# Performance work log

Measured on AMD Instinct MI355X. Metric: run time of the kernel, lower is better.

## Reference

```python
import jax, jax.numpy as jnp
import numpy as np

N, D, HW, FF, DD = 128, 256, 28, 2048, 64
NP_ = D * DD  # num_params = hidden_dim * dim_dynamic = 16384
NH_SELF, NH_ENC = 8, 4


def _conv(x, w, b, stride=1):
    y = jax.lax.conv_general_dilated(x, w, (stride, stride), ((1, 1), (1, 1)),
                                     dimension_numbers=('NCHW', 'OIHW', 'NCHW'))
    return y + b[None, :, None, None]


def _bn(x, g, b):
    # eval-mode BatchNorm2d with running_mean=0, running_var=1
    return x * g[None, :, None, None] + b[None, :, None, None]


def _ln(x, g, b, eps=1e-5):
    m = x.mean(-1, keepdims=True)
    v = ((x - m) ** 2).mean(-1, keepdims=True)
    return (x - m) / jnp.sqrt(v + eps) * g + b


def _mha(x, qkv_w, qkv_b, out_w, out_b, nh):
    # x: (S, B, D) seq-first, like torch MultiheadAttention
    S, B, Dm = x.shape
    dh = Dm // nh
    q, k, v = jnp.split(x @ qkv_w.T + qkv_b, 3, axis=-1)
    q = q.reshape(S, B, nh, dh) * (1.0 / np.sqrt(dh))
    k = k.reshape(S, B, nh, dh)
    v = v.reshape(S, B, nh, dh)
    a = jax.nn.softmax(jnp.einsum('sbhd,tbhd->bhst', q, k), axis=-1)
    o = jnp.einsum('bhst,tbhd->sbhd', a, v).reshape(S, B, Dm)
    return o @ out_w.T + out_b


def _up2(x):
    return jnp.repeat(jnp.repeat(x, 2, axis=2), 2, axis=3)


def _pe(max_len, d):
    pos = jnp.arange(max_len, dtype=jnp.float32)[:, None]
    div = jnp.exp(jnp.arange(0, d, 2, dtype=jnp.float32) * (-np.log(10000.0) / d))
    pe = jnp.zeros((max_len, d), jnp.float32)
    pe = pe.at[:, 0::2].set(jnp.sin(pos * div)).at[:, 1::2].set(jnp.cos(pos * div))
    return pe[:, None, :]  # (max_len, 1, d)


def _forward(roi_features, pro_features, enc_conv_w, enc_conv_b, enc_bn_g, enc_bn_b, attn_qkv_w, attn_qkv_b, attn_out_w, attn_out_b, norm1_g, norm1_b, norm2_g, norm2_b, norm3_g, norm3_b, dyn_w, dyn_b, dnorm1_g, dnorm1_b, dnorm2_g, dnorm2_b, lin1_w, lin1_b, lin2_w, lin2_b, te_qkv_w, te_qkv_b, te_out_w, te_out_b, te_ln1_g, te_ln1_b, te_ln2_g, te_ln2_b, te_ff1_w, te_ff1_b, te_ff2_w, te_ff2_b, rec_conv_w, rec_conv_b, rec_bn_g, rec_bn_b, detA_w, detA_b, det_bnA_g, det_bnA_b, detB_w, detB_b, det_final_w, det_final_b, det_final_bn_g, det_final_bn_b):
    n = roi_features.shape[0]
    h4 = HW // 4
    # ---- k_encoder: two stride-2 conv+BN+ReLU, 28->14->7 ----
    feats_pyr = []
    k = roi_features
    for i in range(2):
        k = jax.nn.relu(_bn(_conv(k, enc_conv_w[i], enc_conv_b[i], stride=2), enc_bn_g[i], enc_bn_b[i]))
        feats_pyr.append(k)
    k = k.reshape(n, D, h4 * h4).transpose(2, 0, 1)  # (49, N, D)
    # ---- self-attention over query tokens ----
    pro = pro_features.reshape(-1, pro_features.shape[-2], D).transpose(1, 0, 2)  # (nq, bs*nf, D)
    pro = _ln(pro + _mha(pro, attn_qkv_w, attn_qkv_b, attn_out_w, attn_out_b, NH_SELF), norm1_g, norm1_b)
    pro = pro.transpose(1, 0, 2).reshape(1, -1, D)  # (1, N, D)
    # ---- DynamicConv_v2 instance interaction ----
    feats = k.transpose(1, 0, 2)  # (N, 49, D)
    params = (pro @ dyn_w.T + dyn_b).transpose(1, 0, 2)  # (N, 1, 2*NP_)
    p1 = params[:, :, :NP_].reshape(-1, D, DD)   # (N, D, 64)
    p2 = params[:, :, NP_:].reshape(-1, DD, D)   # (N, 64, D)
    f = jax.nn.elu(_ln(jnp.einsum('nsc,ncd->nsd', feats, p1), dnorm1_g, dnorm1_b))
    f = jax.nn.elu(_ln(jnp.einsum('nsd,ndc->nsc', f, p2), dnorm2_g, dnorm2_b))  # (N, 49, D)
    pro = feats + f
    obj = _ln(pro, norm2_g, norm2_b)
    # ---- FFN (ELU activation) ----
    obj2 = jax.nn.elu(obj @ lin1_w.T + lin1_b) @ lin2_w.T + lin2_b
    obj = _ln(obj + obj2, norm3_g, norm3_b)
    # ---- pos encoding + 3-layer TransformerEncoder (post-norm, relu, nhead=4) ----
    obj = obj.transpose(1, 0, 2)  # (49, N, D)
    obj = obj + _pe(h4 * h4, D)
    for l in range(3):
        a = _mha(obj, te_qkv_w[l], te_qkv_b[l], te_out_w[l], te_out_b[l], NH_ENC)
        obj = _ln(obj + a, te_ln1_g[l], te_ln1_b[l])
        ff = jax.nn.relu(obj @ te_ff1_w[l].T + te_ff1_b[l]) @ te_ff2_w[l].T + te_ff2_b[l]
        obj = _ln(obj + ff, te_ln2_g[l], te_ln2_b[l])
    obj = obj.transpose(1, 2, 0).reshape(n, D, h4, h4)
    kmap = k.transpose(1, 2, 0).reshape(n, D, h4, h4)
    # ---- gated rec/det decoder pyramid ----
    k_rec = kmap * jax.nn.sigmoid(obj)
    k_rec = jax.nn.relu(_bn(_conv(_up2(k_rec), rec_conv_w[0], rec_conv_b[0]), rec_bn_g[0], rec_bn_b[0])) + feats_pyr[0]
    k_det = _conv(jax.nn.relu(_bn(_conv(_up2(obj), detA_w[0], detA_b[0]), det_bnA_g[0], det_bnA_b[0])), detB_w[0], detB_b[0]) + feats_pyr[0]
    k_rec = k_rec * jax.nn.sigmoid(k_det)
    k_rec = jax.nn.relu(_bn(_conv(_up2(k_rec), rec_conv_w[1], rec_conv_b[1]), rec_bn_g[1], rec_bn_b[1])) + roi_features
    k_det = _conv(jax.nn.relu(_bn(_conv(_up2(k_det), detA_w[1], detA_b[1]), det_bnA_g[1], det_bnA_b[1])), detB_w[1], detB_b[1]) + roi_features
    k_rec = k_rec * jax.nn.sigmoid(k_det)
    # final decoder_layer: Upsample to (28,28) is identity here, then conv+BN+ReLU
    k_rec = jax.nn.relu(_bn(_conv(k_rec, det_final_w, det_final_b), det_final_bn_g, det_final_bn_b))
    return k_rec.reshape(n, D, HW * HW).transpose(0, 2, 1)  # (N, 784, D)


def setup_inputs():
    keys = iter(jax.random.split(jax.random.key(0), 80))
    def rn(shape, s=0.02):
        return jax.random.normal(next(keys), shape, jnp.float32) * s
    d = {
        'roi_features': jax.random.normal(next(keys), (N, D, HW, HW), jnp.float32),
        'pro_features': jax.random.normal(next(keys), (1, 1, N, D), jnp.float32),
        'gt_masks': jax.random.normal(next(keys), (N, HW, HW), jnp.float32),
        'enc_conv_w': rn((2, D, D, 3, 3)), 'enc_conv_b': rn((2, D)),
        'enc_bn_g': jnp.ones((2, D)), 'enc_bn_b': jnp.zeros((2, D)),
        'attn_qkv_w': rn((3 * D, D)), 'attn_qkv_b': rn((3 * D,)),
        'attn_out_w': rn((D, D)), 'attn_out_b': rn((D,)),
        'norm1_g': jnp.ones((D,)), 'norm1_b': jnp.zeros((D,)),
        'norm2_g': jnp.ones((D,)), 'norm2_b': jnp.zeros((D,)),
        'norm3_g': jnp.ones((D,)), 'norm3_b': jnp.zeros((D,)),
        'dyn_w': rn((2 * NP_, D)), 'dyn_b': rn((2 * NP_,)),
        'dnorm1_g': jnp.ones((DD,)), 'dnorm1_b': jnp.zeros((DD,)),
        'dnorm2_g': jnp.ones((D,)), 'dnorm2_b': jnp.zeros((D,)),
        'lin1_w': rn((FF, D)), 'lin1_b': rn((FF,)),
        'lin2_w': rn((D, FF)), 'lin2_b': rn((D,)),
        'te_qkv_w': rn((3, 3 * D, D)), 'te_qkv_b': rn((3, 3 * D)),
        'te_out_w': rn((3, D, D)), 'te_out_b': rn((3, D)),
        'te_ln1_g': jnp.ones((3, D)), 'te_ln1_b': jnp.zeros((3, D)),
        'te_ln2_g': jnp.ones((3, D)), 'te_ln2_b': jnp.zeros((3, D)),
        'te_ff1_w': rn((3, FF, D)), 'te_ff1_b': rn((3, FF)),
        'te_ff2_w': rn((3, D, FF)), 'te_ff2_b': rn((3, D)),
        'rec_conv_w': rn((2, D, D, 3, 3)), 'rec_conv_b': rn((2, D)),
        'rec_bn_g': jnp.ones((2, D)), 'rec_bn_b': jnp.zeros((2, D)),
        'detA_w': rn((2, D, D, 3, 3)), 'detA_b': rn((2, D)),
        'det_bnA_g': jnp.ones((2, D)), 'det_bnA_b': jnp.zeros((2, D)),
        'detB_w': rn((2, D, D, 3, 3)), 'detB_b': rn((2, D)),
        'det_final_w': rn((D, D, 3, 3)), 'det_final_b': rn((D,)),
        'det_final_bn_g': jnp.ones((D,)), 'det_final_bn_b': jnp.zeros((D,)),
    }
    return d


def reference(roi_features, pro_features, gt_masks, enc_conv_w, enc_conv_b, enc_bn_g, enc_bn_b, attn_qkv_w, attn_qkv_b, attn_out_w, attn_out_b, norm1_g, norm1_b, norm2_g, norm2_b, norm3_g, norm3_b, dyn_w, dyn_b, dnorm1_g, dnorm1_b, dnorm2_g, dnorm2_b, lin1_w, lin1_b, lin2_w, lin2_b, te_qkv_w, te_qkv_b, te_out_w, te_out_b, te_ln1_g, te_ln1_b, te_ln2_g, te_ln2_b, te_ff1_w, te_ff1_b, te_ff2_w, te_ff2_b, rec_conv_w, rec_conv_b, rec_bn_g, rec_bn_b, detA_w, detA_b, det_bnA_g, det_bnA_b, detB_w, detB_b, det_final_w, det_final_b, det_final_bn_g, det_final_bn_b):
    # gt_masks is only consumed by the (truncated) SequencePredictor head; unused here
    return _forward(roi_features, pro_features, enc_conv_w, enc_conv_b, enc_bn_g, enc_bn_b, attn_qkv_w, attn_qkv_b, attn_out_w, attn_out_b, norm1_g, norm1_b, norm2_g, norm2_b, norm3_g, norm3_b, dyn_w, dyn_b, dnorm1_g, dnorm1_b, dnorm2_g, dnorm2_b, lin1_w, lin1_b, lin2_w, lin2_b, te_qkv_w, te_qkv_b, te_out_w, te_out_b, te_ln1_g, te_ln1_b, te_ln2_g, te_ln2_b, te_ff1_w, te_ff1_b, te_ff2_w, te_ff2_b, rec_conv_w, rec_conv_b, rec_bn_g, rec_bn_b, detA_w, detA_b, det_bnA_g, det_bnA_b, detB_w, detB_b, det_final_w, det_final_b, det_final_bn_g, det_final_bn_b)
```

## Files before the change

### kernel.cpp

```cpp
#include <hip/hip_runtime.h>
#include <hip/hip_bf16.h>
#include <string.h>

typedef __hip_bfloat16 bf16;
typedef short bf16x8 __attribute__((ext_vector_type(8)));
typedef float f32x16 __attribute__((ext_vector_type(16)));

__device__ __forceinline__ float b2f(bf16 v){ return __bfloat162float(v); }
__device__ __forceinline__ bf16  f2b(float v){ return __float2bfloat16(v); }
__device__ __forceinline__ unsigned short f2bu(float v){
  union { bf16 b; unsigned short u; } x; x.b = __float2bfloat16(v); return x.u;
}
__device__ __forceinline__ float ldf(const float* p, size_t i){ return p[i]; }
__device__ __forceinline__ float ldf(const bf16*  p, size_t i){ return b2f(p[i]); }

__device__ __forceinline__ float2 block_stats256(float x, float* sred){
  float v = x;
  #pragma unroll
  for (int o = 32; o; o >>= 1) v += __shfl_xor(v, o);
  int w = threadIdx.x >> 6;
  if ((threadIdx.x & 63) == 0) sred[w] = v;
  __syncthreads();
  float mean = (sred[0] + sred[1] + sred[2] + sred[3]) * (1.f/256.f);
  __syncthreads();
  float d = x - mean;
  v = d * d;
  #pragma unroll
  for (int o = 32; o; o >>= 1) v += __shfl_xor(v, o);
  if ((threadIdx.x & 63) == 0) sred[w] = v;
  __syncthreads();
  float var = (sred[0] + sred[1] + sred[2] + sred[3]) * (1.f/256.f);
  __syncthreads();
  return make_float2(mean, var);
}

__global__ __launch_bounds__(256) void probe_k(const bf16* __restrict__ buf,
                                               unsigned long long len, float* score){
  __shared__ float sred[4];
  unsigned long long stride = len / 256ull; if (!stride) stride = 1;
  unsigned long long i = (unsigned long long)threadIdx.x * stride;
  if (i >= len) i = len - 1;
  float v = fabsf(b2f(buf[i]));
  #pragma unroll
  for (int o = 32; o; o >>= 1) v = fmaxf(v, __shfl_xor(v, o));
  if ((threadIdx.x & 63) == 0) sred[threadIdx.x >> 6] = v;
  __syncthreads();
  if (threadIdx.x == 0)
    score[0] = fmaxf(fmaxf(sred[0], sred[1]), fmaxf(sred[2], sred[3]));
}

__global__ void verdict_k(const float* score, int nstage, float* out){
  if (threadIdx.x == 0 && blockIdx.x == 0){
    for (int i = 0; i < nstage; i++){
      float s = score[i];
      if (!(s > 1e-8f)){
        float sent = 1000.f + 40.f * i;
        for (int j = 0; j < 64; j++) out[j] = sent;
        return;
      }
    }
  }
}

__global__ __launch_bounds__(256) void troi_k(const float* __restrict__ roi,
                                              bf16* __restrict__ o){
  __shared__ float tile[64][65];
  int n = blockIdx.z, c0 = blockIdx.y * 64, p0 = blockIdx.x * 64;
  int a = threadIdx.x & 63, bq = threadIdx.x >> 6;
  #pragma unroll
  for (int cs = bq; cs < 64; cs += 4){
    int p = p0 + a;
    tile[cs][a] = (p < 784) ? roi[((size_t)n*256 + c0 + cs)*784 + p] : 0.f;
  }
  __syncthreads();
  #pragma unroll
  for (int ps = bq; ps < 64; ps += 4){
    int p = p0 + ps;
    if (p < 784) o[((size_t)n*784 + p)*256 + c0 + a] = f2b(tile[a][ps]);
  }
}

__global__ __launch_bounds__(256) void wtrans_k(const float* __restrict__ w,
                                                bf16* __restrict__ o){
  int co = blockIdx.x, t = threadIdx.x;
  const float* wp = w + (size_t)co * 2304 + (size_t)t * 9;
  #pragma unroll
  for (int tap = 0; tap < 9; tap++)
    o[(size_t)co * 2304 + tap * 256 + t] = f2b(wp[tap]);
}

template<typename T>
__device__ __forceinline__ void stage32(const T* __restrict__ src, bool valid,
                                        char* ldsrow, int ckbase, int swz){
  __align__(16) unsigned short h[32];
  if (valid){
    if constexpr (sizeof(T) == 4){
      #pragma unroll
      for (int i = 0; i < 8; i++){
        float4 f = reinterpret_cast<const float4*>(src)[i];
        h[i*4+0] = f2bu(f.x); h[i*4+1] = f2bu(f.y);
        h[i*4+2] = f2bu(f.z); h[i*4+3] = f2bu(f.w);
      }
    } else {
      #pragma unroll
      for (int i = 0; i < 4; i++)
        reinterpret_cast<uint4*>(h)[i] = reinterpret_cast<const uint4*>(src)[i];
    }
  } else {
    #pragma unroll
    for (int i = 0; i < 4; i++)
      reinterpret_cast<uint4*>(h)[i] = make_uint4(0u,0u,0u,0u);
  }
  #pragma unroll
  for (int i = 0; i < 4; i++)
    *reinterpret_cast<uint4*>(ldsrow + ((ckbase + i*16) ^ swz)) =
        reinterpret_cast<uint4*>(h)[i];
}

__device__ __forceinline__ void mfma_step64(const char* asb, const char* bsb,
                                            int wr, int wc, int lane,
                                            f32x16 (&acc)[2][2]){
  int l31 = lane & 31;
  int lsw = (l31 & 7) << 4;
  int hi  = (lane >> 5) << 4;
  #pragma unroll
  for (int kb = 0; kb < 4; kb++){
    int cb = (kb*32 + hi) ^ lsw;
    bf16x8 a0 = *reinterpret_cast<const bf16x8*>(asb + (wr      + l31)*128 + cb);
    bf16x8 a1 = *reinterpret_cast<const bf16x8*>(asb + (wr + 32 + l31)*128 + cb);
    bf16x8 b0 = *reinterpret_cast<const bf16x8*>(bsb + (wc      + l31)*128 + cb);
    bf16x8 b1 = *reinterpret_cast<const bf16x8*>(bsb + (wc + 32 + l31)*128 + cb);
    acc[0][0] = __builtin_amdgcn_mfma_f32_32x32x16_bf16(a0, b0, acc[0][0], 0, 0, 0);
    acc[0][1] = __builtin_amdgcn_mfma_f32_32x32x16_bf16(a0, b1, acc[0][1], 0, 0, 0);
    acc[1][0] = __builtin_amdgcn_mfma_f32_32x32x16_bf16(a1, b0, acc[1][0], 0, 0, 0);
    acc[1][1] = __builtin_amdgcn_mfma_f32_32x32x16_bf16(a1, b1, acc[1][1], 0, 0, 0);
  }
}

template<int ACT, typename TA>
__global__ __launch_bounds__(256) void gemm_mfma_k(
    const TA* __restrict__ A, const float* __restrict__ W,
    const float* __restrict__ bias, bf16* __restrict__ C,
    int M, int N, int K)
{
  __shared__ __align__(16) unsigned short As[8192];
  __shared__ __align__(16) unsigned short Bs[8192];
  int t = threadIdx.x;
  int n0 = blockIdx.x * 128, m0 = blockIdx.y * 128;
  int lane = t & 63, wave = t >> 6;
  int wr = (wave >> 1) * 64, wc = (wave & 1) * 64;
  int sr = t >> 1, sk = (t & 1) * 32;
  int swz = (sr & 7) << 4;
  char* asb = (char*)As; char* bsb = (char*)Bs;
  char* arow = asb + sr*128; char* brow = bsb + sr*128;
  f32x16 acc[2][2];
  #pragma unroll
  for (int i = 0; i < 2; i++)
    #pragma unroll
    for (int j = 0; j < 2; j++)
      #pragma unroll
      for (int r = 0; r < 16; r++) acc[i][j][r] = 0.f;

  const TA*    ap = A + (size_t)(m0 + sr) * K + sk;
  const float* wp = W + (size_t)(n0 + sr) * K + sk;
  #pragma unroll 1
  for (int k0 = 0; k0 < K; k0 += 64){
    stage32(ap + k0, true, arow, sk*2, swz);
    stage32(wp + k0, true, brow, sk*2, swz);
    __syncthreads();
    mfma_step64(asb, bsb, wr, wc, lane, acc);
    __syncthreads();
  }
  int l31 = lane & 31;
  int rbase = m0 + wr + ((lane >> 5) << 2);
  #pragma unroll
  for (int j = 0; j < 2; j++){
    int n = n0 + wc + j*32 + l31;
    float bv = bias ? bias[n] : 0.f;
    #pragma unroll
    for (int i = 0; i < 2; i++){
      #pragma unroll
      for (int r = 0; r < 16; r++){
        int row = rbase + i*32 + (r & 3) + ((r >> 2) << 3);
        float v = acc[i][j][r] + bv;
        if (ACT == 1) v = fmaxf(v, 0.f);
        if (ACT == 2) v = v > 0.f ? v : (__expf(v) - 1.f);
        C[(size_t)row * N + n] = f2b(v);
      }
    }
  }
}

template<int Ho,int Wo,int Hi,int Wi,int UP2,int STRIDE,
         int HAS_BN,int RELU,int RES_MODE,int GATE,int WOUT,int OUTF>
__global__ __launch_bounds__(256) void conv_mfma_k(
    const bf16* __restrict__ in, const bf16* __restrict__ wTl,
    const float* __restrict__ cbias,
    const float* __restrict__ bng, const float* __restrict__ bnb,
    const void* __restrict__ res, bf16* __restrict__ gate,
    void* __restrict__ out)
{
  constexpr int HWo = Ho * Wo;
  __shared__ __align__(16) unsigned short As[8192];
  __shared__ __align__(16) unsigned short Bs[8192];
  int t = threadIdx.x;
  int co0 = blockIdx.x * 128;
  int gp0 = blockIdx.y * 128;
  int lane = t & 63, wave = t >> 6;
  int wr = (wave >> 1) * 64, wc = (wave & 1) * 64;
  int sr = t >> 1, sk = (t & 1) * 32;
  int swz = (sr & 7) << 4;
  char* asb = (char*)As; char* bsb = (char*)Bs;
  char* arow = asb + sr*128; char* brow = bsb + sr*128;

  int gp = gp0 + sr;
  int n  = gp / HWo;
  int p  = gp - n * HWo;
  int oy = p / Wo, ox = p - oy * Wo;
  const bf16* wrow = wTl + (size_t)(co0 + sr) * 2304;

  f32x16 acc[2][2];
  #pragma unroll
  for (int i = 0; i < 2; i++)
    #pragma unroll
    for (int j = 0; j < 2; j++)
      #pragma unroll
      for (int r = 0; r < 16; r++) acc[i][j][r] = 0.f;

  #pragma unroll 1
  for (int tap = 0; tap < 9; ++tap){
    int ky = tap / 3, kx = tap - ky * 3;
    int iy = oy * STRIDE + ky - 1, ix = ox * STRIDE + kx - 1;
    constexpr int Hv = UP2 ? 2*Hi : Hi;
    constexpr int Wv = UP2 ? 2*Wi : Wi;
    bool val = (iy >= 0) && (iy < Hv) && (ix >= 0) && (ix < Wv);
    int sy = UP2 ? (iy >> 1) : iy;
    int sx = UP2 ? (ix >> 1) : ix;
    if (!val){ sy = 0; sx = 0; }
    const bf16* abase = in + (((size_t)n * Hi + sy) * Wi + sx) * 256;
    const bf16* wbase = wrow + tap * 256;
    #pragma unroll 1
    for (int sub = 0; sub < 4; ++sub){
      stage32(abase + sub*64 + sk, val, arow, sk*2, swz);
      stage32(wbase + sub*64 + sk, true, brow, sk*2, swz);
      __syncthreads();
      mfma_step64(asb, bsb, wr, wc, lane, acc);
      __syncthreads();
    }
  }

  int l31 = lane & 31;
  int rbase = gp0 + wr + ((lane >> 5) << 2);
  #pragma unroll
  for (int j = 0; j < 2; j++){
    int co = co0 + wc + j*32 + l31;
    float cb = cbias[co];
    float scale = 1.f, shift = cb;
    if (HAS_BN){ float g = bng[co]; scale = g; shift = cb*g + bnb[co]; }
    #pragma unroll
    for (int i = 0; i < 2; i++){
      #pragma unroll
      for (int r = 0; r < 16; r++){
        int grow = rbase + i*32 + (r & 3) + ((r >> 2) << 3);
        float v = acc[i][j][r] * scale + shift;
        if (RELU) v = fmaxf(v, 0.f);
        size_t oidx = (size_t)grow * 256 + co;
        if (RES_MODE == 1) v += b2f(((const bf16*)res)[oidx]);
        if (RES_MODE == 2){
          int rn = grow / HWo, rp = grow - rn * HWo;
          v += ((const float*)res)[((size_t)rn * 256 + co) * HWo + rp];
        }
        if (GATE){
          float gv = b2f(gate[oidx]);
          gate[oidx] = f2b(gv / (1.f + __expf(-v)));
        }
        if (WOUT){
          if (OUTF) ((float*)out)[oidx] = v;
          else      ((bf16*)out)[oidx]  = f2b(v);
        }
      }
    }
  }
}

template<int S, int NH, int DH>
__global__ __launch_bounds__(64) void attn_k(
    const bf16* __restrict__ qkv, bf16* __restrict__ out)
{
  const int D = NH * DH;
  int b = blockIdx.x / NH, h = blockIdx.x % NH;
  int chunk = blockIdx.y;
  int lane = threadIdx.x;
  __shared__ float ks[S][DH];
  __shared__ float vs[S][DH];
  __shared__ float os[64][DH];
  for (int idx = lane; idx < S*DH; idx += 64){
    int tt = idx / DH, d = idx % DH;
    size_t row = (size_t)(b*S + tt) * (3*D);
    ks[tt][d] = b2f(qkv[row +   D + h*DH + d]);
    vs[tt][d] = b2f(qkv[row + 2*D + h*DH + d]);
  }
  __syncthreads();
  int s = chunk*64 + lane;
  float q[DH];
  const float scale = 1.f / sqrtf((float)DH);
  if (s < S){
    size_t row = (size_t)(b*S + s) * (3*D);
    #pragma unroll
    for (int d = 0; d < DH; d++) q[d] = b2f(qkv[row + h*DH + d]) * scale;
  } else {
    #pragma unroll
    for (int d = 0; d < DH; d++) q[d] = 0.f;
  }
  float o[DH];
  #pragma unroll
  for (int d = 0; d < DH; d++) o[d] = 0.f;
  float m = -1e30f, l = 0.f;
  for (int tt = 0; tt < S; tt++){
    float sc = 0.f;
    #pragma unroll
    for (int d = 0; d < DH; d++) sc = fmaf(q[d], ks[tt][d], sc);
    float mn = fmaxf(m, sc);
    float corr = __expf(m - mn);
    float e = __expf(sc - mn);
    l = l * corr + e;
    #pragma unroll
    for (int d = 0; d < DH; d++) o[d] = fmaf(o[d], corr, e * vs[tt][d]);
    m = mn;
  }
  float inv = 1.f / l;
  #pragma unroll
  for (int d = 0; d < DH; d++) os[lane][d] = o[d] * inv;
  __syncthreads();
  for (int idx = lane; idx < 64*DH; idx += 64){
    int sl = idx / DH, d = idx % DH;
    int ss = chunk*64 + sl;
    if (ss < S) out[(size_t)(b*S + ss) * D + h*DH + d] = f2b(os[sl][d]);
  }
}

template<int ADD_PE, typename TA>
__global__ __launch_bounds__(256) void add_ln_k(
    const TA* __restrict__ a, const bf16* __restrict__ bsrc,
    const float* __restrict__ g, const float* __restrict__ bb, bf16* out)
{
  __shared__ float sred[4];
  int r = blockIdx.x, c = threadIdx.x;
  size_t idx = (size_t)r * 256 + c;
  float x = ldf(a, idx) + b2f(bsrc[idx]);
  float2 mv = block_stats256(x, sred);
  float y = (x - mv.x) * rsqrtf(mv.y + 1e-5f) * g[c] + bb[c];
  if (ADD_PE){
    int s = r % 49;
    float freq = __expf((float)(c & ~1) * (-9.210340371976184f / 256.f));
    float ang = (float)s * freq;
    y += (c & 1) ? cosf(ang) : sinf(ang);
  }
  out[idx] = f2b(y);
}

__global__ __launch_bounds__(256) void dyn_e1_k(
    const bf16* __restrict__ k2, const bf16* __restrict__ params,
    const float* __restrict__ g, const float* __restrict__ bb,
    bf16* __restrict__ f1)
{
  int n = blockIdx.x;
  int w = threadIdx.x >> 6, d = threadIdx.x & 63;
  const bf16* pp = params + (size_t)n * 32768 + d;
  for (int s = w; s < 49; s += 4){
    const bf16* fp = k2 + ((size_t)n*49 + s) * 256;
    float acc = 0.f;
    #pragma unroll 4
    for (int c = 0; c < 256; c++)
      acc = fmaf(b2f(fp[c]), b2f(pp[c*64]), acc);
    float v = acc;
    #pragma unroll
    for (int o = 32; o; o >>= 1) v += __shfl_xor(v, o);
    float mean = v * (1.f/64.f);
    float dd = acc - mean;
    v = dd * dd;
    #pragma unroll
    for (int o = 32; o; o >>= 1) v += __shfl_xor(v, o);
    float var = v * (1.f/64.f);
    float y = dd * rsqrtf(var + 1e-5f) * g[d] + bb[d];
    y = y > 0.f ? y : (__expf(y) - 1.f);
    f1[((size_t)n*49 + s) * 64 + d] = f2b(y);
  }
}

__global__ __launch_bounds__(256) void dyn_e2_k(
    const bf16* __restrict__ k2, const bf16* __restrict__ params,
    const bf16* __restrict__ f1,
    const float* __restrict__ g2, const float* __restrict__ bb2,
    const float* __restrict__ ng, const float* __restrict__ nb,
    bf16* __restrict__ obj0)
{
  __shared__ float sred[4];
  int ns = blockIdx.x; int n = ns / 49, s = ns % 49;
  int c = threadIdx.x;
  const bf16* pp  = params + (size_t)n * 32768 + 16384 + c;
  const bf16* f1p = f1 + (size_t)ns * 64;
  float acc = 0.f;
  #pragma unroll 8
  for (int d = 0; d < 64; d++)
    acc = fmaf(b2f(f1p[d]), b2f(pp[d*256]), acc);
  float2 mv = block_stats256(acc, sred);
  float y = (acc - mv.x) * rsqrtf(mv.y + 1e-5f) * g2[c] + bb2[c];
  y = y > 0.f ? y : (__expf(y) - 1.f);
  float pro2 = b2f(k2[((size_t)n*49 + s) * 256 + c]) + y;
  float2 mv2 = block_stats256(pro2, sred);
  float y2 = (pro2 - mv2.x) * rsqrtf(mv2.y + 1e-5f) * ng[c] + nb[c];
  obj0[(size_t)ns * 256 + c] = f2b(y2);
}

__global__ __launch_bounds__(256) void gate7_k(
    const bf16* __restrict__ k2, const bf16* __restrict__ obj,
    bf16* __restrict__ rec7)
{
  size_t idx = (size_t)blockIdx.x * 256 + threadIdx.x;
  float ov = b2f(obj[idx]);
  rec7[idx] = f2b(b2f(k2[idx]) / (1.f + __expf(-ov)));
}

extern "C" void kernel_launch(void* const* d_in, const int* in_sizes, int n_in,
                              void* d_out, int out_size, void* d_ws, size_t ws_size,
                              hipStream_t stream)
{
  (void)hipGetLastError();

  static float h_sent[64];
  auto send_sentinel = [&](float val){
    for (int i = 0; i < 64; i++) h_sent[i] = val;
    hipMemcpyAsync(d_out, h_sent, 256, hipMemcpyHostToDevice, stream);
  };

  static const int EXP_SIZES[53] = {
    25690112, 32768, 100352, 1179648, 512, 512, 512, 196608, 768, 65536,
    256, 256, 256, 256, 256, 256, 256, 8388608, 32768, 64,
    64, 256, 256, 524288, 2048, 524288, 256, 589824, 2304, 196608,
    768, 768, 768, 768, 768, 1572864, 6144, 1572864, 768, 1179648,
    512, 512, 512, 1179648, 512, 512, 512, 1179648, 512, 589824,
    256, 256, 256 };
  if (n_in != 53){ send_sentinel(6600.f + (float)n_in); return; }
  for (int i = 0; i < 53; i++)
    if (in_sizes[i] != EXP_SIZES[i]){ send_sentinel(6000.f + 10.f*i); return; }
  if (out_size != 25690112){ send_sentinel(3000.f + (float)(out_size >> 20)); return; }
  if (ws_size < 77070400ull){ send_sentinel(2000.f + (float)(ws_size >> 20)); return; }

  const float* roi    = (const float*)d_in[0];
  const float* proF   = (const float*)d_in[1];
  const float* encW   = (const float*)d_in[3];
  const float* encB   = (const float*)d_in[4];
  const float* encG   = (const float*)d_in[5];
  const float* encBB  = (const float*)d_in[6];
  const float* aqkvW  = (const float*)d_in[7];
  const float* aqkvB  = (const float*)d_in[8];
  const float* aoutW  = (const float*)d_in[9];
  const float* aoutB  = (const float*)d_in[10];
  const float* n1g    = (const float*)d_in[11];
  const float* n1b    = (const float*)d_in[12];
  const float* n2g    = (const float*)d_in[13];
  const float* n2b    = (const float*)d_in[14];
  const float* n3g    = (const float*)d_in[15];
  const float* n3b    = (const float*)d_in[16];
  const float* dynW   = (const float*)d_in[17];
  const float* dynB   = (const float*)d_in[18];
  const float* dn1g   = (const float*)d_in[19];
  const float* dn1b   = (const float*)d_in[20];
  const float* dn2g   = (const float*)d_in[21];
  const float* dn2b   = (const float*)d_in[22];
  const float* lin1W  = (const float*)d_in[23];
  const float* lin1B  = (const float*)d_in[24];
  const float* lin2W  = (const float*)d_in[25];
  const float* lin2B  = (const float*)d_in[26];
  const float* teqkvW = (const float*)d_in[27];
  const float* teqkvB = (const float*)d_in[28];
  const float* teoutW = (const float*)d_in[29];
  const float* teoutB = (const float*)d_in[30];
  const float* teln1g = (const float*)d_in[31];
  const float* teln1b = (const float*)d_in[32];
  const float* teln2g = (const float*)d_in[33];
  const float* teln2b = (const float*)d_in[34];
  const float* teff1W = (const float*)d_in[35];
  const float* teff1B = (const float*)d_in[36];
  const float* teff2W = (const float*)d_in[37];
  const float* teff2B = (const float*)d_in[38];
  const float* recW   = (const float*)d_in[39];
  const float* recB   = (const float*)d_in[40];
  const float* recG   = (const float*)d_in[41];
  const float* recBB  = (const float*)d_in[42];
  const float* dAW    = (const float*)d_in[43];
  const float* dAB    = (const float*)d_in[44];
  const float* dAG    = (const float*)d_in[45];
  const float* dABB   = (const float*)d_in[46];
  const float* dBW    = (const float*)d_in[47];
  const float* dBB_   = (const float*)d_in[48];
  const float* dfW    = (const float*)d_in[49];
  const float* dfB    = (const float*)d_in[50];
  const float* dfG    = (const float*)d_in[51];
  const float* dfBB   = (const float*)d_in[52];

  bf16* base   = (bf16*)d_ws;
  bf16* wT     = base + 0;
  bf16* k1     = base + 5308416;
  bf16* k2     = base + 11730944;
  bf16* qkvP   = base + 13336576;
  bf16* attoP  = base + 13434880;
  bf16* mhaP   = base + 13467648;
  bf16* proQ   = base + 13500416;
  bf16* f1     = base + 13533184;
  bf16* obj0   = base + 13934592;
  bf16* tmp    = base + 15540224;
  bf16* atto   = base + 17145856;
  bf16* obj    = base + 18751488;
  bf16* params = base + 20357120;
  bf16* rec7   = base + 20357120;
  bf16* hbuf   = base + 24551424;
  bf16* qkvT   = base + 24551424;
  bf16* C14    = base + 24551424;
  bf16* B14    = base + 32112640;
  bf16* B28    = base + 5308416;
  bf16* roiT   = (bf16*)d_out;
  bf16* A14    = (bf16*)d_out;
  bf16* C28    = (bf16*)d_out + 6422528;
  float* score = (float*)((char*)d_ws + 77070336);

  troi_k<<<dim3(13,4,128),256,0,stream>>>(roi, roiT);
  wtrans_k<<<256,256,0,stream>>>(encW,            wT + 0*589824);
  wtrans_k<<<256,256,0,stream>>>(encW + 589824,   wT + 1*589824);
  wtrans_k<<<256,256,0,stream>>>(recW,            wT + 2*589824);
  wtrans_k<<<256,256,0,stream>>>(recW + 589824,   wT + 3*589824);
  wtrans_k<<<256,256,0,stream>>>(dAW,             wT + 4*589824);
  wtrans_k<<<256,256,0,stream>>>(dAW + 589824,    wT + 5*589824);
  wtrans_k<<<256,256,0,stream>>>(dBW,             wT + 6*589824);
  wtrans_k<<<256,256,0,stream>>>(dBW + 589824,    wT + 7*589824);
  wtrans_k<<<256,256,0,stream>>>(dfW,             wT + 8*589824);
  probe_k<<<1,256,0,stream>>>(roiT, 25690112ull, score+0);

  conv_mfma_k<14,14,28,28,0,2, 1,1,0,0,1,0><<<dim3(2,196),256,0,stream>>>(
      roiT, wT + 0*589824, encB, encG, encBB, nullptr, nullptr, k1);
  probe_k<<<1,256,0,stream>>>(k1, 6422528ull, score+1);
  conv_mfma_k<7,7,14,14,0,2, 1,1,0,0,1,0><<<dim3(2,49),256,0,stream>>>(
      k1, wT + 1*589824, encB+256, encG+256, encBB+256, nullptr, nullptr, k2);
  probe_k<<<1,256,0,stream>>>(k2, 1605632ull, score+2);

  gemm_mfma_k<0,float><<<dim3(6,1),256,0,stream>>>(proF, aqkvW, aqkvB, qkvP, 128,768,256);
  probe_k<<<1,256,0,stream>>>(qkvP, 98304ull, score+3);
  attn_k<128,8,32><<<dim3(8,2),64,0,stream>>>(qkvP, attoP);
  gemm_mfma_k<0,bf16><<<dim3(2,1),256,0,stream>>>(attoP, aoutW, aoutB, mhaP, 128,256,256);
  add_ln_k<0,float><<<128,256,0,stream>>>(proF, mhaP, n1g, n1b, proQ);
  probe_k<<<1,256,0,stream>>>(proQ, 32768ull, score+4);

  gemm_mfma_k<0,bf16><<<dim3(256,1),256,0,stream>>>(proQ, dynW, dynB, params, 128,32768,256);
  probe_k<<<1,256,0,stream>>>(params, 4194304ull, score+5);
  dyn_e1_k<<<128,256,0,stream>>>(k2, params, dn1g, dn1b, f1);
  probe_k<<<1,256,0,stream>>>(f1, 401408ull, score+6);
  dyn_e2_k<<<6272,256,0,stream>>>(k2, params, f1, dn2g, dn2b, n2g, n2b, obj0);
  probe_k<<<1,256,0,stream>>>(obj0, 1605632ull, score+7);

  gemm_mfma_k<2,bf16><<<dim3(16,49),256,0,stream>>>(obj0, lin1W, lin1B, hbuf, 6272,2048,256);
  gemm_mfma_k<0,bf16><<<dim3(2,49),256,0,stream>>>(hbuf, lin2W, lin2B, tmp, 6272,256,2048);
  add_ln_k<1,bf16><<<6272,256,0,stream>>>(obj0, tmp, n3g, n3b, obj);
  probe_k<<<1,256,0,stream>>>(obj, 1605632ull, score+8);

  for (int l = 0; l < 3; l++){
    gemm_mfma_k<0,bf16><<<dim3(6,49),256,0,stream>>>(
        obj, teqkvW + (size_t)l*196608, teqkvB + l*768, qkvT, 6272,768,256);
    attn_k<49,4,64><<<dim3(512,1),64,0,stream>>>(qkvT, atto);
    gemm_mfma_k<0,bf16><<<dim3(2,49),256,0,stream>>>(
        atto, teoutW + (size_t)l*65536, teoutB + l*256, tmp, 6272,256,256);
    add_ln_k<0,bf16><<<6272,256,0,stream>>>(obj, tmp, teln1g + l*256, teln1b + l*256, obj);
    gemm_mfma_k<1,bf16><<<dim3(16,49),256,0,stream>>>(
        obj, teff1W + (size_t)l*524288, teff1B + l*2048, hbuf, 6272,2048,256);
    gemm_mfma_k<0,bf16><<<dim3(2,49),256,0,stream>>>(
        hbuf, teff2W + (size_t)l*524288, teff2B + l*256, tmp, 6272,256,2048);
    add_ln_k<0,bf16><<<6272,256,0,stream>>>(obj, tmp, teln2g + l*256, teln2b + l*256, obj);
  }
  probe_k<<<1,256,0,stream>>>(obj, 1605632ull, score+9);

  gate7_k<<<6272,256,0,stream>>>(k2, obj, rec7);
  probe_k<<<1,256,0,stream>>>(rec7, 1605632ull, score+10);
  conv_mfma_k<14,14,7,7,1,1, 1,1,1,0,1,0><<<dim3(2,196),256,0,stream>>>(
      rec7, wT + 2*589824, recB, recG, recBB, k1, nullptr, B14);
  probe_k<<<1,256,0,stream>>>(B14, 6422528ull, score+11);
  conv_mfma_k<14,14,7,7,1,1, 1,1,0,0,1,0><<<dim3(2,196),256,0,stream>>>(
      obj, wT + 4*589824, dAB, dAG, dABB, nullptr, nullptr, C14);
  conv_mfma_k<14,14,14,14,0,1, 0,0,1,1,1,0><<<dim3(2,196),256,0,stream>>>(
      C14, wT + 6*589824, dBB_, nullptr, nullptr, k1, B14, A14);
  probe_k<<<1,256,0,stream>>>(A14, 6422528ull, score+12);
  conv_mfma_k<28,28,14,14,1,1, 1,1,2,0,1,0><<<dim3(2,784),256,0,stream>>>(
      B14, wT + 3*589824, recB+256, recG+256, recBB+256, roi, nullptr, B28);
  probe_k<<<1,256,0,stream>>>(B28, 25690112ull, score+13);
  conv_mfma_k<28,28,14,14,1,1, 1,1,0,0,1,0><<<dim3(2,784),256,0,stream>>>(
      A14, wT + 5*589824, dAB+256, dAG+256, dABB+256, nullptr, nullptr, C28);
  conv_mfma_k<28,28,28,28,0,1, 0,0,2,1,0,0><<<dim3(2,784),256,0,stream>>>(
      C28, wT + 7*589824, dBB_+256, nullptr, nullptr, roi, B28, nullptr);
  conv_mfma_k<28,28,28,28,0,1, 1,1,0,0,1,1><<<dim3(2,784),256,0,stream>>>(
      B28, wT + 8*589824, dfB, dfG, dfBB, nullptr, nullptr, d_out);

  verdict_k<<<1,64,0,stream>>>(score, 14, (float*)d_out);
  hipError_t le = hipGetLastError();
  if (le != hipSuccess){
    float v = 7000.f + 16.f * (float)(int)le;
    if (v > 60000.f) v = 60000.f;
    send_sentinel(v);
  }
}
```

Before: 2.517 ms.

## Double-buffer LDS with register prefetch and XCD-aware block swizzle in MFMA GEMM/conv

Converts the GEMM and implicit-GEMM conv main loops to a double-buffered LDS scheme. The next K-slice is loaded into registers before the MFMA step on the current buffer, then written to the other buffer. Block indices are remapped so consecutive tiles land on the same XCD for better L2 reuse, and launch bounds request 2 blocks per CU. The cost is double the LDS footprint (64KB per block), which may limit occupancy, plus extra register pressure from the prefetch registers.

```diff
diff --git a/kernel.cpp b/kernel.cpp
--- a/kernel.cpp
+++ b/kernel.cpp
@@ -13,6 +13,35 @@
 }
 __device__ __forceinline__ float ldf(const float* p, size_t i){ return p[i]; }
 __device__ __forceinline__ float ldf(const bf16*  p, size_t i){ return b2f(p[i]); }
+
+__device__ __forceinline__ int xcd_swizzle(int lin, int nwg){
+  int q = nwg >> 3, r = nwg & 7;
+  int x = lin & 7, i = lin >> 3;
+  int base = (x < r) ? x * (q + 1) : r * (q + 1) + (x - r) * q;
+  return base + i;
+}
+
+template<typename T>
+__device__ __forceinline__ void load32(const T* __restrict__ p, bool val, uint4 (&h)[4]){
+  if (!val){
+    #pragma unroll
+    for (int i = 0; i < 4; i++) h[i] = make_uint4(0u,0u,0u,0u);
+    return;
+  }
+  if constexpr (sizeof(T) == 4){
+    #pragma unroll
+    for (int i = 0; i < 8; i++){
+      float4 f = reinterpret_cast<const float4*>(p)[i];
+      unsigned int lo = (unsigned int)f2bu(f.x) | ((unsigned int)f2bu(f.y) << 16);
+      unsigned int hi = (unsigned int)f2bu(f.z) | ((unsigned int)f2bu(f.w) << 16);
+      if ((i & 1) == 0){ h[i>>1].x = lo; h[i>>1].y = hi; }
+      else             { h[i>>1].z = lo; h[i>>1].w = hi; }
+    }
+  } else {
+    #pragma unroll
+    for (int i = 0; i < 4; i++) h[i] = reinterpret_cast<const uint4*>(p)[i];
+  }
+}
 
 __device__ __forceinline__ float2 block_stats256(float x, float* sred){
   float v = x;
@@ -89,34 +118,6 @@
     o[(size_t)co * 2304 + tap * 256 + t] = f2b(wp[tap]);
 }
 
-template<typename T>
-__device__ __forceinline__ void stage32(const T* __restrict__ src, bool valid,
-                                        char* ldsrow, int ckbase, int swz){
-  __align__(16) unsigned short h[32];
-  if (valid){
-    if constexpr (sizeof(T) == 4){
-      #pragma unroll
-      for (int i = 0; i < 8; i++){
-        float4 f = reinterpret_cast<const float4*>(src)[i];
-        h[i*4+0] = f2bu(f.x); h[i*4+1] = f2bu(f.y);
-        h[i*4+2] = f2bu(f.z); h[i*4+3] = f2bu(f.w);
-      }
-    } else {
-      #pragma unroll
-      for (int i = 0; i < 4; i++)
-        reinterpret_cast<uint4*>(h)[i] = reinterpret_cast<const uint4*>(src)[i];
-    }
-  } else {
-    #pragma unroll
-    for (int i = 0; i < 4; i++)
-      reinterpret_cast<uint4*>(h)[i] = make_uint4(0u,0u,0u,0u);
-  }
-  #pragma unroll
-  for (int i = 0; i < 4; i++)
-    *reinterpret_cast<uint4*>(ldsrow + ((ckbase + i*16) ^ swz)) =
-        reinterpret_cast<uint4*>(h)[i];
-}
-
 __device__ __forceinline__ void mfma_step64(const char* asb, const char* bsb,
                                             int wr, int wc, int lane,
                                             f32x16 (&acc)[2][2]){
@@ -138,21 +139,22 @@
 }
 
 template<int ACT, typename TA>
-__global__ __launch_bounds__(256) void gemm_mfma_k(
+__global__ __launch_bounds__(256,2) void gemm_mfma_k(
     const TA* __restrict__ A, const float* __restrict__ W,
     const float* __restrict__ bias, bf16* __restrict__ C,
     int M, int N, int K)
 {
-  __shared__ __align__(16) unsigned short As[8192];
-  __shared__ __align__(16) unsigned short Bs[8192];
+  __shared__ __align__(16) unsigned short As[2][8192];
+  __shared__ __align__(16) unsigned short Bs[2][8192];
   int t = threadIdx.x;
-  int n0 = blockIdx.x * 128, m0 = blockIdx.y * 128;
+  int nbx = gridDim.x;
+  int lin = blockIdx.y * nbx + blockIdx.x;
+  int wg  = xcd_swizzle(lin, nbx * gridDim.y);
+  int n0 = (wg % nbx) * 128, m0 = (wg / nbx) * 128;
   int lane = t & 63, wave = t >> 6;
   int wr = (wave >> 1) * 64, wc = (wave & 1) * 64;
   int sr = t >> 1, sk = (t & 1) * 32;
   int swz = (sr & 7) << 4;
-  char* asb = (char*)As; char* bsb = (char*)Bs;
-  char* arow = asb + sr*128; char* brow = bsb + sr*128;
   f32x16 acc[2][2];
   #pragma unroll
   for (int i = 0; i < 2; i++)
@@ -163,14 +165,35 @@
 
   const TA*    ap = A + (size_t)(m0 + sr) * K + sk;
   const float* wp = W + (size_t)(n0 + sr) * K + sk;
+  uint4 ha[4], hb[4];
+
+  auto commit = [&](int buf){
+    char* ar = (char*)As[buf] + sr*128;
+    char* br = (char*)Bs[buf] + sr*128;
+    #pragma unroll
+    for (int i = 0; i < 4; i++){
+      *reinterpret_cast<uint4*>(ar + ((sk*2 + i*16) ^ swz)) = ha[i];
+      *reinterpret_cast<uint4*>(br + ((sk*2 + i*16) ^ swz)) = hb[i];
+    }
+  };
+
+  int NIT = K >> 6;
+  load32(ap, true, ha);
+  load32(wp, true, hb);
+  commit(0);
+  __syncthreads();
   #pragma unroll 1
-  for (int k0 = 0; k0 < K; k0 += 64){
-    stage32(ap + k0, true, arow, sk*2, swz);
-    stage32(wp + k0, true, brow, sk*2, swz);
+  for (int it = 0; it < NIT; ++it){
+    if (it + 1 < NIT){
+      load32(ap + (size_t)(it+1)*64, true, ha);
+      load32(wp + (size_t)(it+1)*64, true, hb);
+    }
+    mfma_step64((const char*)As[it&1], (const char*)Bs[it&1], wr, wc, lane, acc);
     __syncthreads();
-    mfma_step64(asb, bsb, wr, wc, lane, acc);
+    if (it + 1 < NIT) commit((it+1)&1);
     __syncthreads();
   }
+
   int l31 = lane & 31;
   int rbase = m0 + wr + ((lane >> 5) << 2);
   #pragma unroll
@@ -193,7 +216,7 @@
 
 template<int Ho,int Wo,int Hi,int Wi,int UP2,int STRIDE,
          int HAS_BN,int RELU,int RES_MODE,int GATE,int WOUT,int OUTF>
-__global__ __launch_bounds__(256) void conv_mfma_k(
+__global__ __launch_bounds__(256,2) void conv_mfma_k(
     const bf16* __restrict__ in, const bf16* __restrict__ wTl,
     const float* __restrict__ cbias,
     const float* __restrict__ bng, const float* __restrict__ bnb,
@@ -201,17 +224,20 @@
     void* __restrict__ out)
 {
   constexpr int HWo = Ho * Wo;
-  __shared__ __align__(16) unsigned short As[8192];
-  __shared__ __align__(16) unsigned short Bs[8192];
+  constexpr int Hv = UP2 ? 2*Hi : Hi;
+  constexpr int Wv = UP2 ? 2*Wi : Wi;
+  __shared__ __align__(16) unsigned short As[2][8192];
+  __shared__ __align__(16) unsigned short Bs[2][8192];
   int t = threadIdx.x;
-  int co0 = blockIdx.x * 128;
-  int gp0 = blockIdx.y * 128;
+  int nbx = gridDim.x;
+  int lin = blockIdx.y * nbx + blockIdx.x;
+  int wg  = xcd_swizzle(lin, nbx * gridDim.y);
+  int co0 = (wg % nbx) * 128;
+  int gp0 = (wg / nbx) * 128;
   int lane = t & 63, wave = t >> 6;
   int wr = (wave >> 1) * 64, wc = (wave & 1) * 64;
   int sr = t >> 1, sk = (t & 1) * 32;
   int swz = (sr & 7) << 4;
-  char* asb = (char*)As; char* bsb = (char*)Bs;
-  char* arow = asb + sr*128; char* brow = bsb + sr*128;
 
   int gp = gp0 + sr;
   int n  = gp / HWo;
@@ -227,26 +253,39 @@
       #pragma unroll
       for (int r = 0; r < 16; r++) acc[i][j][r] = 0.f;
 
-  #pragma unroll 1
-  for (int tap = 0; tap < 9; ++tap){
+  uint4 ha[4], hb[4];
+  auto issue = [&](int it){
+    int tap = it >> 2, sub = it & 3;
     int ky = tap / 3, kx = tap - ky * 3;
     int iy = oy * STRIDE + ky - 1, ix = ox * STRIDE + kx - 1;
-    constexpr int Hv = UP2 ? 2*Hi : Hi;
-    constexpr int Wv = UP2 ? 2*Wi : Wi;
     bool val = (iy >= 0) && (iy < Hv) && (ix >= 0) && (ix < Wv);
     int sy = UP2 ? (iy >> 1) : iy;
     int sx = UP2 ? (ix >> 1) : ix;
     if (!val){ sy = 0; sx = 0; }
-    const bf16* abase = in + (((size_t)n * Hi + sy) * Wi + sx) * 256;
-    const bf16* wbase = wrow + tap * 256;
-    #pragma unroll 1
-    for (int sub = 0; sub < 4; ++sub){
-      stage32(abase + sub*64 + sk, val, arow, sk*2, swz);
-      stage32(wbase + sub*64 + sk, true, brow, sk*2, swz);
-      __syncthreads();
-      mfma_step64(asb, bsb, wr, wc, lane, acc);
-      __syncthreads();
+    const bf16* ap = in + (((size_t)n * Hi + sy) * Wi + sx) * 256 + sub*64 + sk;
+    const bf16* bp = wrow + tap * 256 + sub*64 + sk;
+    load32(ap, val, ha);
+    load32(bp, true, hb);
+  };
+  auto commit = [&](int buf){
+    char* ar = (char*)As[buf] + sr*128;
+    char* br = (char*)Bs[buf] + sr*128;
+    #pragma unroll
+    for (int i = 0; i < 4; i++){
+      *reinterpret_cast<uint4*>(ar + ((sk*2 + i*16) ^ swz)) = ha[i];
+      *reinterpret_cast<uint4*>(br + ((sk*2 + i*16) ^ swz)) = hb[i];
     }
+  };
+
+  issue(0); commit(0);
+  __syncthreads();
+  #pragma unroll 1
+  for (int it = 0; it < 36; ++it){
+    if (it + 1 < 36) issue(it + 1);
+    mfma_step64((const char*)As[it&1], (const char*)Bs[it&1], wr, wc, lane, acc);
+    __syncthreads();
+    if (it + 1 < 36) commit((it+1)&1);
+    __syncthreads();
   }
 
   int l31 = lane & 31;
```

Result: slower. 2.924 ms (+16.2%).
